# Kernel optimization log

Measured on AMD Instinct MI355X. Metric: run time of the kernel, lower is better.

Reference implementation:

```python
import jax, jax.numpy as jnp
import numpy as np

# constants matching CombinedLoss_dynamic(a=1.0, alpha=0.0257, source_intensity=1e5)
ALPHA = 0.0257
A = 1.0
NORM = 27353.34765625
SRC_INTENSITY = 100000.0 / NORM
FIRE_THRESHOLD = (1000.0 - 20.0) / NORM


def _laplace_kernel():
    # 7-point 3D Laplacian stencil, shape [1,1,3,3,3] (OIDHW)
    k = jnp.zeros((3, 3, 3), dtype=jnp.float32)
    k = k.at[1, 1, 1].set(-6.0)
    k = k.at[0, 1, 1].set(1.0).at[2, 1, 1].set(1.0)
    k = k.at[1, 0, 1].set(1.0).at[1, 2, 1].set(1.0)
    k = k.at[1, 1, 0].set(1.0).at[1, 1, 2].set(1.0)
    return k[None, None]


def _laplacian3d(x):
    # x: [B, 1, D, H, W]; groups = C = 1, zero padding 1 on each spatial dim
    kernel = _laplace_kernel().astype(x.dtype)
    return jax.lax.conv_general_dilated(
        x, kernel,
        window_strides=(1, 1, 1),
        padding=[(1, 1), (1, 1), (1, 1)],
        dimension_numbers=("NCDHW", "OIDHW", "NCDHW"),
    )


def setup_inputs() -> dict:
    key = jax.random.key(0)
    ks = jax.random.split(key, 4)
    B, C, D, H, W = 16, 1, 64, 128, 128
    shape = (B, C, D, H, W)
    return {
        "input": jax.random.normal(ks[0], shape, dtype=jnp.float32),
        "output": jax.random.normal(ks[1], shape, dtype=jnp.float32),
        "output_past": jax.random.normal(ks[2], shape, dtype=jnp.float32),
        "t": jnp.ones((B, C), dtype=jnp.float32),
        "t_past": jnp.zeros((B, C), dtype=jnp.float32),
        "target": jax.random.normal(ks[3], shape, dtype=jnp.float32),
    }


def reference(input, output, output_past, t, t_past, target):
    # temporal derivative: (out - out_past) / (t - t_past), t broadcast over DHW
    dt = (t - t_past)[:, :, None, None, None]  # [B,1,1,1,1]
    temporal_derivative = (output - output_past) / dt
    laplacian = _laplacian3d(input)
    source_term = jnp.where(input > FIRE_THRESHOLD,
                            jnp.float32(SRC_INTENSITY), jnp.float32(0.0))
    residual = temporal_derivative - ALPHA * laplacian - source_term
    p_loss = jnp.mean(residual * residual)
    mse = jnp.mean((output - target) ** 2)
    return mse + A * p_loss
```

## Files before the change

kernel.cpp:

```cpp
#include <hip/hip_runtime.h>

typedef float f4 __attribute__((ext_vector_type(4)));

#define NORMC 27353.34765625f
#define ALPHA_C 0.0257f
#define SRC_INTENSITY (100000.0f / NORMC)
#define FIRE_THRESHOLD (980.0f / NORMC)

constexpr int Wd = 128, Hd = 128, Dd = 64, Bd = 16;
constexpr int W4 = Wd / 4;
constexpr int HW4 = (Hd * Wd) / 4;
constexpr long long NTOT = (long long)Bd * Dd * Hd * Wd;
constexpr int N4 = (int)(NTOT / 4);
constexpr int NBLK = 2048;
constexpr int NTH = 256;
constexpr int STRIDE4 = NBLK * NTH;
constexpr int NITER = N4 / STRIDE4;

__device__ __forceinline__ f4 ldg4(const float* p) { return *(const f4*)p; }

__global__ __launch_bounds__(NTH, 8) void loss_main(
    const float* __restrict__ in,
    const float* __restrict__ outc,
    const float* __restrict__ outp,
    const float* __restrict__ tvec,
    const float* __restrict__ tpvec,
    const float* __restrict__ tgt,
    float2* __restrict__ partial)
{
    const int tid  = threadIdx.x;
    const int base = blockIdx.x * NTH + tid;

    const int x4    = tid & (W4 - 1);
    const bool xl_ok = (x4 > 0);
    const bool xr_ok = (x4 < W4 - 1);

    float sp = 0.0f;
    float sm = 0.0f;

    #pragma unroll 2
    for (int k = 0; k < NITER; ++k) {
        const int i4  = base + k * STRIDE4;
        const int idx = i4 << 2;
        const int y   = (i4 >> 5) & (Hd - 1);
        const int z   = (i4 >> 12) & (Dd - 1);
        const int b   = i4 >> 18;

        const f4 zero4 = {0.f, 0.f, 0.f, 0.f};
        const f4 c = ldg4(in + idx);
        const f4 ym = (y > 0)      ? ldg4(in + idx - Wd)         : zero4;
        const f4 yp = (y < Hd - 1) ? ldg4(in + idx + Wd)         : zero4;
        const f4 zm = (z > 0)      ? ldg4(in + idx - (HW4 << 2)) : zero4;
        const f4 zp = (z < Dd - 1) ? ldg4(in + idx + (HW4 << 2)) : zero4;
        const f4 o  = ldg4(outc + idx);
        const f4 op = ldg4(outp + idx);
        const f4 tg = ldg4(tgt  + idx);

        const float xls = __shfl_up(c.w, 1);
        const float xrs = __shfl_down(c.x, 1);
        const float xl  = xl_ok ? xls : 0.0f;
        const float xr  = xr_ok ? xrs : 0.0f;

        const float dt  = tvec[b] - tpvec[b];
        const float rdt = 1.0f / dt;

        const float lap0 = xl  + c.y + ym.x + yp.x + zm.x + zp.x - 6.0f * c.x;
        const float lap1 = c.x + c.z + ym.y + yp.y + zm.y + zp.y - 6.0f * c.y;
        const float lap2 = c.y + c.w + ym.z + yp.z + zm.z + zp.z - 6.0f * c.z;
        const float lap3 = c.z + xr  + ym.w + yp.w + zm.w + zp.w - 6.0f * c.w;

        const float src0 = (c.x > FIRE_THRESHOLD) ? SRC_INTENSITY : 0.0f;
        const float src1 = (c.y > FIRE_THRESHOLD) ? SRC_INTENSITY : 0.0f;
        const float src2 = (c.z > FIRE_THRESHOLD) ? SRC_INTENSITY : 0.0f;
        const float src3 = (c.w > FIRE_THRESHOLD) ? SRC_INTENSITY : 0.0f;

        const float r0 = (o.x - op.x) * rdt - ALPHA_C * lap0 - src0;
        const float r1 = (o.y - op.y) * rdt - ALPHA_C * lap1 - src1;
        const float r2 = (o.z - op.z) * rdt - ALPHA_C * lap2 - src2;
        const float r3 = (o.w - op.w) * rdt - ALPHA_C * lap3 - src3;
        sp += r0 * r0 + r1 * r1 + r2 * r2 + r3 * r3;

        const float m0 = o.x - tg.x, m1 = o.y - tg.y;
        const float m2 = o.z - tg.z, m3 = o.w - tg.w;
        sm += m0 * m0 + m1 * m1 + m2 * m2 + m3 * m3;
    }

    #pragma unroll
    for (int off = 32; off > 0; off >>= 1) {
        sp += __shfl_down(sp, off);
        sm += __shfl_down(sm, off);
    }
    __shared__ float2 wsum[NTH / 64];
    const int lane = tid & 63;
    const int wid  = tid >> 6;
    if (lane == 0) wsum[wid] = make_float2(sp, sm);
    __syncthreads();
    if (tid == 0) {
        float ap = 0.0f, am = 0.0f;
        #pragma unroll
        for (int w = 0; w < NTH / 64; ++w) { ap += wsum[w].x; am += wsum[w].y; }
        partial[blockIdx.x] = make_float2(ap, am);
    }
}

__global__ __launch_bounds__(256) void loss_reduce(
    const float2* __restrict__ partial, float* __restrict__ out)
{
    double sp = 0.0, sm = 0.0;
    for (int i = threadIdx.x; i < NBLK; i += blockDim.x) {
        const float2 v = partial[i];
        sp += (double)v.x;
        sm += (double)v.y;
    }
    #pragma unroll
    for (int off = 32; off > 0; off >>= 1) {
        sp += __shfl_down(sp, off);
        sm += __shfl_down(sm, off);
    }
    __shared__ double wsp[4], wsm[4];
    const int lane = threadIdx.x & 63;
    const int wid  = threadIdx.x >> 6;
    if (lane == 0) { wsp[wid] = sp; wsm[wid] = sm; }
    __syncthreads();
    if (threadIdx.x == 0) {
        double tp = 0.0, tm = 0.0;
        #pragma unroll
        for (int w = 0; w < 4; ++w) { tp += wsp[w]; tm += wsm[w]; }
        const double invN = 1.0 / (double)NTOT;
        out[0] = (float)(tm * invN + tp * invN);
    }
}

extern "C" void kernel_launch(void* const* d_in, const int* in_sizes, int n_in,
                              void* d_out, int out_size, void* d_ws, size_t ws_size,
                              hipStream_t stream) {
    const float* in_   = (const float*)d_in[0];
    const float* out_  = (const float*)d_in[1];
    const float* outp_ = (const float*)d_in[2];
    const float* t_    = (const float*)d_in[3];
    const float* tp_   = (const float*)d_in[4];
    const float* tgt_  = (const float*)d_in[5];

    float2* partial = (float2*)d_ws;

    loss_main<<<NBLK, NTH, 0, stream>>>(in_, out_, outp_, t_, tp_, tgt_, partial);
    loss_reduce<<<1, 256, 0, stream>>>(partial, (float*)d_out);
}
```

Measured before the change: 56.19 us.

## Double-buffer streamed inputs through LDS with async global_load_lds prefetch

The four contiguous streams (input centre, output, output_past, target) are now prefetched one iteration ahead, straight into a double-buffered LDS array via global_load_lds, with manual vmcnt/lgkmcnt waits. The stencil neighbours are still loaded directly from global memory. The goal is to overlap HBM latency with compute in a memory-bound kernel. It adds LDS usage and fragile hand-written waitcnt logic; the vmcnt(4) wait assumes the neighbour loads are ordered with the prefetches, and dropping the occupancy hint may change register allocation.

```diff
diff --git a/kernel.cpp b/kernel.cpp
--- a/kernel.cpp
+++ b/kernel.cpp
@@ -9,17 +9,21 @@
 
 constexpr int Wd = 128, Hd = 128, Dd = 64, Bd = 16;
 constexpr int W4 = Wd / 4;
-constexpr int HW4 = (Hd * Wd) / 4;
 constexpr long long NTOT = (long long)Bd * Dd * Hd * Wd;
 constexpr int N4 = (int)(NTOT / 4);
 constexpr int NBLK = 2048;
 constexpr int NTH = 256;
+constexpr int NWAVES = NTH / 64;
 constexpr int STRIDE4 = NBLK * NTH;
 constexpr int NITER = N4 / STRIDE4;
+constexpr int HWc = Hd * Wd;
+
+typedef const __attribute__((address_space(1))) unsigned int* gasp;
+typedef __attribute__((address_space(3))) unsigned int* lasp;
 
 __device__ __forceinline__ f4 ldg4(const float* p) { return *(const f4*)p; }
 
-__global__ __launch_bounds__(NTH, 8) void loss_main(
+__global__ __launch_bounds__(NTH) void loss_main(
     const float* __restrict__ in,
     const float* __restrict__ outc,
     const float* __restrict__ outp,
@@ -28,12 +32,24 @@
     const float* __restrict__ tgt,
     float2* __restrict__ partial)
 {
+    __shared__ f4 lds4[2][NWAVES][4][64];
+
     const int tid  = threadIdx.x;
+    const int lane = tid & 63;
+    const int wid  = tid >> 6;
     const int base = blockIdx.x * NTH + tid;
 
-    const int x4    = tid & (W4 - 1);
+    const int x4     = tid & (W4 - 1);
     const bool xl_ok = (x4 > 0);
     const bool xr_ok = (x4 < W4 - 1);
+
+    {
+        const int idx = base << 2;
+        __builtin_amdgcn_global_load_lds((gasp)(in   + idx), (lasp)&lds4[0][wid][0][0], 16, 0, 0);
+        __builtin_amdgcn_global_load_lds((gasp)(outc + idx), (lasp)&lds4[0][wid][1][0], 16, 0, 0);
+        __builtin_amdgcn_global_load_lds((gasp)(outp + idx), (lasp)&lds4[0][wid][2][0], 16, 0, 0);
+        __builtin_amdgcn_global_load_lds((gasp)(tgt  + idx), (lasp)&lds4[0][wid][3][0], 16, 0, 0);
+    }
 
     float sp = 0.0f;
     float sm = 0.0f;
@@ -45,16 +61,33 @@
         const int y   = (i4 >> 5) & (Hd - 1);
         const int z   = (i4 >> 12) & (Dd - 1);
         const int b   = i4 >> 18;
+        const int cur = k & 1;
+
+        asm volatile("s_waitcnt lgkmcnt(0)" ::: "memory");
+
+        if (k < NITER - 1) {
+            const int nidx = idx + (STRIDE4 << 2);
+            const int nb   = cur ^ 1;
+            __builtin_amdgcn_global_load_lds((gasp)(in   + nidx), (lasp)&lds4[nb][wid][0][0], 16, 0, 0);
+            __builtin_amdgcn_global_load_lds((gasp)(outc + nidx), (lasp)&lds4[nb][wid][1][0], 16, 0, 0);
+            __builtin_amdgcn_global_load_lds((gasp)(outp + nidx), (lasp)&lds4[nb][wid][2][0], 16, 0, 0);
+            __builtin_amdgcn_global_load_lds((gasp)(tgt  + nidx), (lasp)&lds4[nb][wid][3][0], 16, 0, 0);
+            asm volatile("s_waitcnt vmcnt(4)" ::: "memory");
+        } else {
+            asm volatile("s_waitcnt vmcnt(0)" ::: "memory");
+        }
+        __builtin_amdgcn_sched_barrier(0);
+
+        const f4 c  = lds4[cur][wid][0][lane];
+        const f4 o  = lds4[cur][wid][1][lane];
+        const f4 op = lds4[cur][wid][2][lane];
+        const f4 tg = lds4[cur][wid][3][lane];
 
         const f4 zero4 = {0.f, 0.f, 0.f, 0.f};
-        const f4 c = ldg4(in + idx);
-        const f4 ym = (y > 0)      ? ldg4(in + idx - Wd)         : zero4;
-        const f4 yp = (y < Hd - 1) ? ldg4(in + idx + Wd)         : zero4;
-        const f4 zm = (z > 0)      ? ldg4(in + idx - (HW4 << 2)) : zero4;
-        const f4 zp = (z < Dd - 1) ? ldg4(in + idx + (HW4 << 2)) : zero4;
-        const f4 o  = ldg4(outc + idx);
-        const f4 op = ldg4(outp + idx);
-        const f4 tg = ldg4(tgt  + idx);
+        const f4 ym = (y > 0)      ? ldg4(in + idx - Wd)  : zero4;
+        const f4 yp = (y < Hd - 1) ? ldg4(in + idx + Wd)  : zero4;
+        const f4 zm = (z > 0)      ? ldg4(in + idx - HWc) : zero4;
+        const f4 zp = (z < Dd - 1) ? ldg4(in + idx + HWc) : zero4;
 
         const float xls = __shfl_up(c.w, 1);
         const float xrs = __shfl_down(c.x, 1);
@@ -90,15 +123,13 @@
         sp += __shfl_down(sp, off);
         sm += __shfl_down(sm, off);
     }
-    __shared__ float2 wsum[NTH / 64];
-    const int lane = tid & 63;
-    const int wid  = tid >> 6;
+    __shared__ float2 wsum[NWAVES];
     if (lane == 0) wsum[wid] = make_float2(sp, sm);
     __syncthreads();
     if (tid == 0) {
         float ap = 0.0f, am = 0.0f;
         #pragma unroll
-        for (int w = 0; w < NTH / 64; ++w) { ap += wsum[w].x; am += wsum[w].y; }
+        for (int w = 0; w < NWAVES; ++w) { ap += wsum[w].x; am += wsum[w].y; }
         partial[blockIdx.x] = make_float2(ap, am);
     }
 }
```

Result: faster. 50.15 us (-10.7%).
